# Kernel optimization log

Hardware: AMD Instinct MI355X
Metric: run time of the kernel (lower is better)

Reference implementation:

```python
import jax, jax.numpy as jnp
import numpy as np

B, P, C, O = 16, 19248, 81, 32
POS_THRESH, NEG_THRESH, NEGPOS_RATIO = 0.5, 0.4, 3
BBOX_ALPHA, CONF_ALPHA = 1.5, 1.0
VAR0, VAR1 = 0.1, 0.2  # SSD encoding variances


def setup_inputs() -> dict:
    key = jax.random.key(0)
    ks = jax.random.split(key, 7)
    loc_data = jax.random.normal(ks[0], (B, P, 4), dtype=jnp.float32)
    conf_data = jax.random.normal(ks[1], (B, P, C), dtype=jnp.float32)
    # priors in center form (cx, cy, w, h), all positive
    cxcy = jax.random.uniform(ks[2], (P, 2), minval=0.05, maxval=0.95)
    wh = jax.random.uniform(ks[3], (P, 2), minval=0.05, maxval=0.30)
    priors = jnp.concatenate([cxcy, wh], axis=-1).astype(jnp.float32)
    # gt boxes in point form (x1, y1, x2, y2), valid and inside [0,1]
    gcxcy = jax.random.uniform(ks[4], (B, O, 2), minval=0.1, maxval=0.9)
    gwh = jax.random.uniform(ks[5], (B, O, 2), minval=0.05, maxval=0.4)
    gt_boxes = jnp.clip(jnp.concatenate([gcxcy - gwh / 2, gcxcy + gwh / 2], axis=-1), 0.0, 1.0).astype(jnp.float32)
    gt_labels = jax.random.randint(ks[6], (B, O), 0, C - 1, dtype=jnp.int32)  # 0..79, bg is class 0 after +1
    return {"loc_data": loc_data, "conf_data": conf_data, "priors": priors,
            "gt_boxes": gt_boxes, "gt_labels": gt_labels}


def _point_form(boxes):
    # center form (cx,cy,w,h) -> point form (x1,y1,x2,y2)
    return jnp.concatenate([boxes[:, :2] - boxes[:, 2:] / 2,
                            boxes[:, :2] + boxes[:, 2:] / 2], axis=-1)


def _jaccard(a, b):
    # a: [O,4] point form, b: [P,4] point form -> IoU [O,P]
    lt = jnp.maximum(a[:, None, :2], b[None, :, :2])
    rb = jnp.minimum(a[:, None, 2:], b[None, :, 2:])
    inter = jnp.prod(jnp.clip(rb - lt, 0.0, None), axis=-1)
    area_a = jnp.prod(a[:, 2:] - a[:, :2], axis=-1)[:, None]
    area_b = jnp.prod(b[:, 2:] - b[:, :2], axis=-1)[None, :]
    return inter / (area_a + area_b - inter)


def _encode(matched, priors):
    # matched: [P,4] point form gt; priors: [P,4] center form
    g_cxcy = ((matched[:, :2] + matched[:, 2:]) / 2 - priors[:, :2]) / (VAR0 * priors[:, 2:])
    g_wh = jnp.log((matched[:, 2:] - matched[:, :2]) / priors[:, 2:]) / VAR1
    return jnp.concatenate([g_cxcy, g_wh], axis=-1)


def _match_one(truths, labels, priors):
    # truths: [O,4] point form, labels: [O] int, priors: [P,4] center form
    overlaps = _jaccard(truths, _point_form(priors))          # [O,P]
    best_truth_overlap = overlaps.max(axis=0)                  # [P]
    best_truth_idx = overlaps.argmax(axis=0)                   # [P]
    best_prior_idx = overlaps.argmax(axis=1)                   # [O]
    # ensure every gt is matched to its best prior
    best_truth_overlap = best_truth_overlap.at[best_prior_idx].set(2.0)
    best_truth_idx = best_truth_idx.at[best_prior_idx].set(jnp.arange(truths.shape[0]))
    matched = truths[best_truth_idx]                           # [P,4]
    conf = labels[best_truth_idx] + 1                          # [P]
    conf = jnp.where(best_truth_overlap < POS_THRESH, -1, conf)  # neutral
    conf = jnp.where(best_truth_overlap < NEG_THRESH, 0, conf)   # background
    loc = _encode(matched, priors)                             # [P,4]
    return loc, conf


def _multibox_loss(loc_data, conf_data, priors, gt_boxes, gt_labels):
    loc_t, conf_t = jax.vmap(_match_one, in_axes=(0, 0, None))(gt_boxes, gt_labels, priors)
    pos = conf_t > 0                                           # [B,P]
    # --- localization: smooth L1 on positives ---
    d = jnp.abs(loc_data - loc_t)
    sl1 = jnp.where(d < 1.0, 0.5 * d * d, d - 0.5)
    loss_B = jnp.sum(sl1 * pos[..., None].astype(sl1.dtype)) * BBOX_ALPHA
    # --- OHEM confidence loss ---
    logZ = jax.nn.logsumexp(conf_data, axis=-1)                # [B,P]
    loss_c = logZ - conf_data[..., 0]                          # log_sum_exp - background logit
    loss_c = jnp.where(pos | (conf_t < 0), 0.0, loss_c)
    order = jnp.argsort(-loss_c, axis=1)                       # descending
    idx_rank = jnp.argsort(order, axis=1)                      # rank of each prior
    num_pos = jnp.sum(pos, axis=1, keepdims=True)              # [B,1]
    num_neg = jnp.clip(NEGPOS_RATIO * num_pos, None, P - 1)
    neg = (idx_rank < num_neg) & (~pos) & (conf_t >= 0)
    ce = logZ - jnp.take_along_axis(conf_data, jnp.maximum(conf_t, 0)[..., None], axis=-1)[..., 0]
    loss_C = jnp.sum(ce * (pos | neg).astype(ce.dtype)) * CONF_ALPHA
    total_num_pos = jnp.sum(pos).astype(loc_data.dtype)
    return jnp.stack([loss_B, loss_C]) / total_num_pos


def reference(loc_data, conf_data, priors, gt_boxes, gt_labels):
    return _multibox_loss(loc_data, conf_data, priors, gt_boxes, gt_labels)
```

## Files before the change

### kernel.cpp

```cpp
#include <hip/hip_runtime.h>
#include <math.h>

#define B_ 16
#define P_ 19248
#define C_ 81
#define O_ 32
#define POS_TH 0.5f
#define NEG_TH 0.4f
#define RPB 128
#define TPB 512
#define PQ  4812
#define BP_BLK (B_ * O_ * 4)
#define BT_BPB 76
#define NJ 38

__device__ __forceinline__ float sl1(float x) {
    float d = fabsf(x);
    return (d < 1.0f) ? 0.5f * d * d : d - 0.5f;
}

__device__ __forceinline__ float iou_gt_prior(float4 t, float4 pr) {
    float px1 = pr.x - pr.z * 0.5f;
    float py1 = pr.y - pr.w * 0.5f;
    float px2 = pr.x + pr.z * 0.5f;
    float py2 = pr.y + pr.w * 0.5f;
    float ltx = fmaxf(t.x, px1), lty = fmaxf(t.y, py1);
    float rbx = fminf(t.z, px2), rby = fminf(t.w, py2);
    float iw = fmaxf(rbx - ltx, 0.0f), ih = fmaxf(rby - lty, 0.0f);
    float inter = iw * ih;
    float area_t = (t.z - t.x) * (t.w - t.y);
    float area_p = (px2 - px1) * (py2 - py1);
    return inter / (area_t + area_p - inter);
}

template <int PER>
__device__ __forceinline__ void pick_top(const int* __restrict__ h, int kk, int tid,
                                         int* s_bin, int* s_kk, int* wsum) {
    const int lane = tid & 63, wid = tid >> 6;
    const int base = tid * PER;
    int v[PER]; int s = 0;
    #pragma unroll
    for (int j = 0; j < PER; ++j) { v[j] = h[base + j]; s += v[j]; }
    int x = s;
    #pragma unroll
    for (int d = 1; d < 64; d <<= 1) {
        int y = __shfl_down(x, d);
        if (lane + d < 64) x += y;
    }
    if (lane == 0) wsum[wid] = x;
    __syncthreads();
    int above = 0;
    #pragma unroll
    for (int w = 0; w < 8; ++w) if (w > wid) above += wsum[w];
    int T = (x - s) + above;
    if (T < kk && kk <= T + s) {
        int kl = kk - T, cum = 0;
        #pragma unroll
        for (int j = PER - 1; j >= 0; --j) {
            if (cum + v[j] >= kl) { *s_bin = base + j; *s_kk = kl - cum; break; }
            cum += v[j];
        }
    }
    __syncthreads();
}

template <int PER>
__device__ __forceinline__ void pick_bot(const int* __restrict__ h, int kk, int tid,
                                         int* s_bin, int* s_kk, int* wsum) {
    const int lane = tid & 63, wid = tid >> 6;
    const int base = tid * PER;
    int v[PER]; int s = 0;
    #pragma unroll
    for (int j = 0; j < PER; ++j) { v[j] = h[base + j]; s += v[j]; }
    int x = s;
    #pragma unroll
    for (int d = 1; d < 64; d <<= 1) {
        int y = __shfl_up(x, d);
        if (lane >= d) x += y;
    }
    if (lane == 63) wsum[wid] = x;
    __syncthreads();
    int below = 0;
    #pragma unroll
    for (int w = 0; w < 8; ++w) if (w < wid) below += wsum[w];
    int T = (x - s) + below;
    if (T < kk && kk <= T + s) {
        int kl = kk - T, cum = 0;
        #pragma unroll
        for (int j = 0; j < PER; ++j) {
            if (cum + v[j] >= kl) { *s_bin = base + j; *s_kk = kl - cum; break; }
            cum += v[j];
        }
    }
    __syncthreads();
}

__global__ void k_match(const float* __restrict__ priors,
                        const float* __restrict__ gt_boxes,
                        const int* __restrict__ gt_labels,
                        unsigned long long* __restrict__ best_key,
                        float* __restrict__ bt_ov,
                        int* __restrict__ bt_ix,
                        int* __restrict__ bt_lab) {
    const int bid = blockIdx.x;
    if (bid < BP_BLK) {
        int pair = bid >> 2, qtr = bid & 3;
        int b = pair >> 5, o = pair & 31;
        float4 t = ((const float4*)gt_boxes)[b * O_ + o];
        float bestv = -1.0f; int besti = 0;
        int pstart = qtr * PQ;
        for (int p = pstart + threadIdx.x; p < pstart + PQ; p += 256) {
            float4 pr = ((const float4*)priors)[p];
            float v = iou_gt_prior(t, pr);
            if (v > bestv) { bestv = v; besti = p; }
        }
        __shared__ float sv[256];
        __shared__ int   si[256];
        sv[threadIdx.x] = bestv; si[threadIdx.x] = besti;
        __syncthreads();
        for (int s = 128; s > 0; s >>= 1) {
            if (threadIdx.x < s) {
                float ov = sv[threadIdx.x + s]; int oi = si[threadIdx.x + s];
                if (ov > sv[threadIdx.x] ||
                    (ov == sv[threadIdx.x] && oi < si[threadIdx.x])) {
                    sv[threadIdx.x] = ov; si[threadIdx.x] = oi;
                }
            }
            __syncthreads();
        }
        if (threadIdx.x == 0) {
            unsigned long long key =
                ((unsigned long long)__float_as_uint(sv[0]) << 32) |
                (unsigned long long)(0xFFFFFFFFu - (unsigned int)si[0]);
            atomicMax(&best_key[pair], key);
        }
    } else {
        int idx = bid - BP_BLK;
        int b = idx / BT_BPB;
        int p = (idx % BT_BPB) * 256 + threadIdx.x;
        __shared__ float4 gt[O_];
        __shared__ int    gl[O_];
        if (threadIdx.x < O_) {
            gt[threadIdx.x] = ((const float4*)gt_boxes)[b * O_ + threadIdx.x];
            gl[threadIdx.x] = gt_labels[b * O_ + threadIdx.x];
        }
        __syncthreads();
        if (p >= P_) return;
        float4 pr = ((const float4*)priors)[p];
        float bestv = -1.0f; int besti = 0;
        for (int o = 0; o < O_; ++o) {
            float v = iou_gt_prior(gt[o], pr);
            if (v > bestv) { bestv = v; besti = o; }
        }
        size_t bp = (size_t)b * P_ + p;
        bt_ov[bp] = bestv;
        bt_ix[bp] = besti;
        bt_lab[bp] = gl[besti];
    }
}

__global__ void k_force(const unsigned long long* __restrict__ best_key,
                        const int* __restrict__ gt_labels,
                        float* __restrict__ bt_ov,
                        int* __restrict__ bt_ix,
                        int* __restrict__ bt_lab,
                        int* __restrict__ num_pos,
                        float* __restrict__ accum,
                        int* __restrict__ done) {
    const int tid = threadIdx.x;
    const int b = tid >> 5, o = tid & 31;
    unsigned long long key = best_key[b * O_ + o];
    int p  = (int)(0xFFFFFFFFu - (unsigned int)(key & 0xFFFFFFFFu));
    int ll = gt_labels[b * O_ + o];
    if (tid < B_) num_pos[tid] = 0;
    if (tid == 0) { accum[0] = 0.0f; accum[1] = 0.0f; *done = 0; }
    const int lanebase = tid & 32;
    for (int oo = 0; oo < O_; ++oo) {
        int pp = __shfl(p, lanebase + oo);
        int l2 = __shfl(ll, lanebase + oo);
        if (o == 0) {
            size_t idx = (size_t)b * P_ + pp;
            bt_ov[idx] = 2.0f;
            bt_ix[idx] = oo;
            bt_lab[idx] = l2;
        }
    }
}

__global__ __launch_bounds__(TPB, 6) void
k_main(const float* __restrict__ loc_data,
       const float* __restrict__ conf_data,
       const float* __restrict__ priors,
       const float* __restrict__ gt_boxes,
       const float* __restrict__ bt_ov,
       const int* __restrict__ bt_ix,
       const int* __restrict__ bt_lab,
       float* __restrict__ lossc,
       float* __restrict__ ce_neg,
       int* __restrict__ num_pos,
       float* __restrict__ accum) {
    __shared__ float srow[RPB * C_];
    __shared__ float s_lB, s_ceP;
    __shared__ int s_np0, s_np1;
    const int row0 = blockIdx.x * RPB;
    const int tid = threadIdx.x;
    const int w = tid >> 6;
    if (tid == 0) { s_lB = 0.0f; s_ceP = 0.0f; s_np0 = 0; s_np1 = 0; }

    {
        const float4* src = (const float4*)(conf_data + (size_t)row0 * C_);
        float4* dst4 = (float4*)srow;
        #pragma unroll
        for (int k = 0; k < 5; ++k) {
            __builtin_amdgcn_global_load_lds(
                (const __attribute__((address_space(1))) void*)(src + k * 512 + tid),
                (__attribute__((address_space(3))) void*)(dst4 + k * 512 + (w << 6)),
                16, 0, 0);
        }
        if (tid < 32) {
            __builtin_amdgcn_global_load_lds(
                (const __attribute__((address_space(1))) void*)(src + 2560 + tid),
                (__attribute__((address_space(3))) void*)(dst4 + 2560),
                16, 0, 0);
        }
    }
    __syncthreads();

    const int r = tid >> 2;
    const int q = tid & 3;
    const int bp = row0 + r;
    const int b = bp / P_;
    const int b0 = row0 / P_;
    const int p = bp - b * P_;
    const float* row = srow + r * C_;
    const int j0 = 20 * q;

    float ma = row[j0], mb = row[j0 + 1], mc = row[j0 + 2], md = row[j0 + 3];
    #pragma unroll
    for (int i = 4; i < 20; i += 4) {
        ma = fmaxf(ma, row[j0 + i]);     mb = fmaxf(mb, row[j0 + i + 1]);
        mc = fmaxf(mc, row[j0 + i + 2]); md = fmaxf(md, row[j0 + i + 3]);
    }
    float m = fmaxf(fmaxf(ma, mb), fmaxf(mc, md));
    if (q == 3) m = fmaxf(m, row[80]);
    m = fmaxf(m, __shfl_xor(m, 1));
    m = fmaxf(m, __shfl_xor(m, 2));

    float sa = 0.f, sb = 0.f, sc = 0.f, sd = 0.f;
    #pragma unroll
    for (int i = 0; i < 20; i += 4) {
        sa += __expf(row[j0 + i] - m);     sb += __expf(row[j0 + i + 1] - m);
        sc += __expf(row[j0 + i + 2] - m); sd += __expf(row[j0 + i + 3] - m);
    }
    float s = (sa + sb) + (sc + sd);
    if (q == 3) s += __expf(row[80] - m);
    s += __shfl_xor(s, 1);
    s += __shfl_xor(s, 2);
    float logZ = m + __logf(s);

    if (q == 0) {
        float ov = bt_ov[bp];
        int lab = bt_lab[bp];
        int conf_t = lab + 1;
        if (ov < POS_TH) conf_t = -1;
        if (ov < NEG_TH) conf_t = 0;
        bool pos = conf_t > 0;

        float lc = (pos || conf_t < 0) ? 0.0f : (logZ - row[0]);
        int cls = pos ? conf_t : 0;
        float ce = logZ - row[cls];

        lossc[bp] = lc;
        ce_neg[bp] = (conf_t == 0) ? ce : 0.0f;

        if (pos) {
            int ti = bt_ix[bp];
            float4 t = ((const float4*)gt_boxes)[b * O_ + ti];
            float4 pr = ((const float4*)priors)[p];
            float mcx = (t.x + t.z) * 0.5f;
            float mcy = (t.y + t.w) * 0.5f;
            float gx = (mcx - pr.x) / (0.1f * pr.z);
            float gy = (mcy - pr.y) / (0.1f * pr.w);
            float gw = logf((t.z - t.x) / pr.z) / 0.2f;
            float gh = logf((t.w - t.y) / pr.w) / 0.2f;
            float4 ld = ((const float4*)loc_data)[bp];
            float sc2 = sl1(ld.x - gx) + sl1(ld.y - gy) + sl1(ld.z - gw) + sl1(ld.w - gh);
            atomicAdd(&s_lB, sc2);
            atomicAdd(&s_ceP, ce);
            if (b == b0) atomicAdd(&s_np0, 1); else atomicAdd(&s_np1, 1);
        }
    }
    __syncthreads();
    if (tid == 0) {
        if (s_lB != 0.0f) atomicAdd(&accum[0], s_lB);
        if (s_ceP != 0.0f) atomicAdd(&accum[1], s_ceP);
        if (s_np0) atomicAdd(&num_pos[b0], s_np0);
        if (s_np1) atomicAdd(&num_pos[b0 + 1], s_np1);
    }
}

__global__ __launch_bounds__(512) void
k_ohem(const float* __restrict__ lossc, const float* __restrict__ ce_neg,
       const int* __restrict__ num_pos, const float* __restrict__ accum,
       float* __restrict__ ce_sum, int* __restrict__ done,
       float* __restrict__ out) {
    const int b = blockIdx.x;
    const int tid = threadIdx.x;
    const float* lc = lossc + (size_t)b * P_;
    const float* cn = ce_neg + (size_t)b * P_;
    __shared__ int h[2048];
    __shared__ int wsum[8];
    __shared__ int s_bin, s_kk;
    __shared__ float red[512];

    int k = 3 * num_pos[b];
    if (k > P_ - 1) k = P_ - 1;

    float result = 0.0f;
    if (k > 0) {
        unsigned int fb[NJ]; float cv[NJ];
        #pragma unroll
        for (int j = 0; j < NJ; ++j) {
            int i = tid + j * 512;
            bool valid = (i < P_);
            fb[j] = valid ? __float_as_uint(lc[i]) : 0xFFFFFFFFu;
            cv[j] = valid ? cn[i] : 0.0f;
        }
        for (int i = tid; i < 2048; i += 512) h[i] = 0;
        __syncthreads();
        #pragma unroll
        for (int j = 0; j < NJ; ++j) atomicAdd(&h[fb[j] >> 21], 1);
        __syncthreads();
        pick_top<2>(h, k, tid, &s_bin, &s_kk, wsum);
        const unsigned int T = (unsigned int)s_bin;
        int kk = s_kk;

        for (int i = tid; i < 2048; i += 512) h[i] = 0;
        __syncthreads();
        float sum = 0.0f;
        #pragma unroll
        for (int j = 0; j < NJ; ++j) {
            unsigned int bin = fb[j] >> 21;
            if (bin > T) sum += cv[j];
            else if (bin == T) atomicAdd(&h[(fb[j] >> 10) & 2047], 1);
        }
        __syncthreads();
        pick_top<4>(h, kk, tid, &s_bin, &s_kk, wsum);
        const unsigned int pre21 = (T << 11) | (unsigned int)s_bin;
        kk = s_kk;

        for (int i = tid; i < 1024; i += 512) h[i] = 0;
        __syncthreads();
        #pragma unroll
        for (int j = 0; j < NJ; ++j)
            if ((fb[j] >> 10) == pre21) atomicAdd(&h[fb[j] & 1023], 1);
        __syncthreads();
        pick_top<2>(h, kk, tid, &s_bin, &s_kk, wsum);
        const unsigned int V = (pre21 << 10) | (unsigned int)s_bin;
        const int ee = h[s_bin];
        kk = s_kk;

        if (kk == ee) {
            #pragma unroll
            for (int j = 0; j < NJ; ++j)
                if ((fb[j] >> 21) == T && fb[j] >= V) sum += cv[j];
        } else {
            for (int i = tid; i < 512; i += 512) h[i] = 0;
            __syncthreads();
            #pragma unroll
            for (int j = 0; j < NJ; ++j)
                if (fb[j] == V) atomicAdd(&h[(tid + j * 512) >> 6], 1);
            __syncthreads();
            pick_bot<1>(h, kk, tid, &s_bin, &s_kk, wsum);
            const int d6 = s_bin;
            kk = s_kk;
            h[tid] = 0;
            __syncthreads();
            #pragma unroll
            for (int j = 0; j < NJ; ++j) {
                int i = tid + j * 512;
                if (fb[j] == V && (i >> 6) == d6) atomicAdd(&h[i & 63], 1);
            }
            __syncthreads();
            pick_bot<1>(h, kk, tid, &s_bin, &s_kk, wsum);
            const int Istar = (d6 << 6) | s_bin;
            #pragma unroll
            for (int j = 0; j < NJ; ++j) {
                int i = tid + j * 512;
                if ((fb[j] >> 21) == T && (fb[j] > V || (fb[j] == V && i <= Istar)))
                    sum += cv[j];
            }
        }

        red[tid] = sum;
        __syncthreads();
        for (int s = 256; s > 0; s >>= 1) {
            if (tid < s) red[tid] += red[tid + s];
            __syncthreads();
        }
        result = red[0];
    }

    if (tid == 0) {
        ce_sum[b] = result;
        __threadfence();
        int old = atomicAdd(done, 1);
        if (old == B_ - 1) {
            __threadfence();
            int tp = 0; float ns = 0.0f;
            for (int bb = 0; bb < B_; ++bb) { tp += num_pos[bb]; ns += ce_sum[bb]; }
            float inv = 1.0f / (float)tp;
            out[0] = accum[0] * 1.5f * inv;
            out[1] = (accum[1] + ns) * inv;
        }
    }
}

extern "C" void kernel_launch(void* const* d_in, const int* in_sizes, int n_in,
                              void* d_out, int out_size, void* d_ws, size_t ws_size,
                              hipStream_t stream) {
    const float* loc    = (const float*)d_in[0];
    const float* conf   = (const float*)d_in[1];
    const float* priors = (const float*)d_in[2];
    const float* gtb    = (const float*)d_in[3];
    const int*   gtl    = (const int*)d_in[4];
    float* out = (float*)d_out;

    const size_t BP = (size_t)B_ * P_;
    float* W = (float*)d_ws;
    float* bt_ov   = W;
    float* lossc   = W + BP;
    float* ce_neg  = W + 2 * BP;
    int*   bt_ix   = (int*)(W + 3 * BP);
    int*   bt_lab  = (int*)(W + 4 * BP);
    unsigned long long* best_key = (unsigned long long*)(W + 5 * BP);
    int*   num_pos = (int*)(best_key + B_ * O_);
    float* ce_sum  = (float*)(num_pos + B_);
    float* accum   = ce_sum + B_;
    int*   done    = (int*)(accum + 2);

    hipMemsetAsync(best_key, 0, B_ * O_ * sizeof(unsigned long long), stream);
    hipLaunchKernelGGL(k_match, dim3(BP_BLK + B_ * BT_BPB), dim3(256), 0, stream,
                       priors, gtb, gtl, best_key, bt_ov, bt_ix, bt_lab);
    hipLaunchKernelGGL(k_force, dim3(1), dim3(512), 0, stream,
                       best_key, gtl, bt_ov, bt_ix, bt_lab, num_pos, accum, done);
    hipLaunchKernelGGL(k_main, dim3((int)(BP / RPB)), dim3(TPB), 0, stream,
                       loc, conf, priors, gtb, bt_ov, bt_ix, bt_lab,
                       lossc, ce_neg, num_pos, accum);
    hipLaunchKernelGGL(k_ohem, dim3(B_), dim3(512), 0, stream,
                       lossc, ce_neg, num_pos, accum, ce_sum, done, out);
}
```

Baseline: 119.9 us.

## Fold forced-match kernel into main kernel and widen OHEM select to 1024 threads

Removes the single-block k_force launch. Each k_main block now loads the per-GT best-prior indices and labels for its batch rows into shared memory and applies the forced matches itself. The zeroing of num_pos, accum and done moves into the existing memset. k_ohem now uses 1024 threads with half the per-thread register arrays, and the radix-select histograms and scans are adjusted to match. This saves a serial kernel launch and doubles parallelism in the OHEM selection, at the cost of a 32-entry shared-memory scan per row in k_main and more barrier participants in k_ohem.

```diff
diff --git a/kernel.cpp b/kernel.cpp
--- a/kernel.cpp
+++ b/kernel.cpp
@@ -12,7 +12,8 @@
 #define PQ  4812
 #define BP_BLK (B_ * O_ * 4)
 #define BT_BPB 76
-#define NJ 38
+#define OT 1024
+#define NJ 19
 
 __device__ __forceinline__ float sl1(float x) {
     float d = fabsf(x);
@@ -51,7 +52,7 @@
     __syncthreads();
     int above = 0;
     #pragma unroll
-    for (int w = 0; w < 8; ++w) if (w > wid) above += wsum[w];
+    for (int w = 0; w < 16; ++w) if (w > wid) above += wsum[w];
     int T = (x - s) + above;
     if (T < kk && kk <= T + s) {
         int kl = kk - T, cum = 0;
@@ -82,7 +83,7 @@
     __syncthreads();
     int below = 0;
     #pragma unroll
-    for (int w = 0; w < 8; ++w) if (w < wid) below += wsum[w];
+    for (int w = 0; w < 16; ++w) if (w < wid) below += wsum[w];
     int T = (x - s) + below;
     if (T < kk && kk <= T + s) {
         int kl = kk - T, cum = 0;
@@ -159,39 +160,13 @@
     }
 }
 
-__global__ void k_force(const unsigned long long* __restrict__ best_key,
-                        const int* __restrict__ gt_labels,
-                        float* __restrict__ bt_ov,
-                        int* __restrict__ bt_ix,
-                        int* __restrict__ bt_lab,
-                        int* __restrict__ num_pos,
-                        float* __restrict__ accum,
-                        int* __restrict__ done) {
-    const int tid = threadIdx.x;
-    const int b = tid >> 5, o = tid & 31;
-    unsigned long long key = best_key[b * O_ + o];
-    int p  = (int)(0xFFFFFFFFu - (unsigned int)(key & 0xFFFFFFFFu));
-    int ll = gt_labels[b * O_ + o];
-    if (tid < B_) num_pos[tid] = 0;
-    if (tid == 0) { accum[0] = 0.0f; accum[1] = 0.0f; *done = 0; }
-    const int lanebase = tid & 32;
-    for (int oo = 0; oo < O_; ++oo) {
-        int pp = __shfl(p, lanebase + oo);
-        int l2 = __shfl(ll, lanebase + oo);
-        if (o == 0) {
-            size_t idx = (size_t)b * P_ + pp;
-            bt_ov[idx] = 2.0f;
-            bt_ix[idx] = oo;
-            bt_lab[idx] = l2;
-        }
-    }
-}
-
 __global__ __launch_bounds__(TPB, 6) void
 k_main(const float* __restrict__ loc_data,
        const float* __restrict__ conf_data,
        const float* __restrict__ priors,
        const float* __restrict__ gt_boxes,
+       const int* __restrict__ gt_labels,
+       const unsigned long long* __restrict__ best_key,
        const float* __restrict__ bt_ov,
        const int* __restrict__ bt_ix,
        const int* __restrict__ bt_lab,
@@ -200,9 +175,12 @@
        int* __restrict__ num_pos,
        float* __restrict__ accum) {
     __shared__ float srow[RPB * C_];
+    __shared__ int s_fp[2][O_];
+    __shared__ int s_fl[2][O_];
     __shared__ float s_lB, s_ceP;
     __shared__ int s_np0, s_np1;
     const int row0 = blockIdx.x * RPB;
+    const int b0 = row0 / P_;
     const int tid = threadIdx.x;
     const int w = tid >> 6;
     if (tid == 0) { s_lB = 0.0f; s_ceP = 0.0f; s_np0 = 0; s_np1 = 0; }
@@ -224,13 +202,24 @@
                 16, 0, 0);
         }
     }
+    if (tid < 2 * O_) {
+        int half = tid >> 5, o = tid & 31;
+        int bb = b0 + half;
+        int fp = -1, fl = 0;
+        if (bb < B_) {
+            unsigned long long key = best_key[bb * O_ + o];
+            fp = (int)(0xFFFFFFFFu - (unsigned int)(key & 0xFFFFFFFFu));
+            fl = gt_labels[bb * O_ + o];
+        }
+        s_fp[half][o] = fp;
+        s_fl[half][o] = fl;
+    }
     __syncthreads();
 
     const int r = tid >> 2;
     const int q = tid & 3;
     const int bp = row0 + r;
     const int b = bp / P_;
-    const int b0 = row0 / P_;
     const int p = bp - b * P_;
     const float* row = srow + r * C_;
     const int j0 = 20 * q;
@@ -259,12 +248,26 @@
     float logZ = m + __logf(s);
 
     if (q == 0) {
-        float ov = bt_ov[bp];
-        int lab = bt_lab[bp];
-        int conf_t = lab + 1;
-        if (ov < POS_TH) conf_t = -1;
-        if (ov < NEG_TH) conf_t = 0;
-        bool pos = conf_t > 0;
+        const int whichb = b - b0;
+        int foo = -1;
+        #pragma unroll
+        for (int oo = O_ - 1; oo >= 0; --oo) {
+            if (foo < 0 && s_fp[whichb][oo] == p) foo = oo;
+        }
+        int conf_t, ti = 0;
+        bool pos;
+        if (foo >= 0) {
+            conf_t = s_fl[whichb][foo] + 1;
+            pos = true;
+            ti = foo;
+        } else {
+            float ov = bt_ov[bp];
+            conf_t = bt_lab[bp] + 1;
+            if (ov < POS_TH) conf_t = -1;
+            if (ov < NEG_TH) conf_t = 0;
+            pos = conf_t > 0;
+            if (pos) ti = bt_ix[bp];
+        }
 
         float lc = (pos || conf_t < 0) ? 0.0f : (logZ - row[0]);
         int cls = pos ? conf_t : 0;
@@ -274,7 +277,6 @@
         ce_neg[bp] = (conf_t == 0) ? ce : 0.0f;
 
         if (pos) {
-            int ti = bt_ix[bp];
             float4 t = ((const float4*)gt_boxes)[b * O_ + ti];
             float4 pr = ((const float4*)priors)[p];
             float mcx = (t.x + t.z) * 0.5f;
@@ -299,7 +301,7 @@
     }
 }
 
-__global__ __launch_bounds__(512) void
+__global__ __launch_bounds__(OT) void
 k_ohem(const float* __restrict__ lossc, const float* __restrict__ ce_neg,
        const int* __restrict__ num_pos, const float* __restrict__ accum,
        float* __restrict__ ce_sum, int* __restrict__ done,
@@ -309,9 +311,9 @@
     const float* lc = lossc + (size_t)b * P_;
     const float* cn = ce_neg + (size_t)b * P_;
     __shared__ int h[2048];
-    __shared__ int wsum[8];
+    __shared__ int wsum[16];
     __shared__ int s_bin, s_kk;
-    __shared__ float red[512];
+    __shared__ float red[OT];
 
     int k = 3 * num_pos[b];
     if (k > P_ - 1) k = P_ - 1;
@@ -321,12 +323,12 @@
         unsigned int fb[NJ]; float cv[NJ];
         #pragma unroll
         for (int j = 0; j < NJ; ++j) {
-            int i = tid + j * 512;
+            int i = tid + j * OT;
             bool valid = (i < P_);
-            fb[j] = valid ? __float_as_uint(lc[i]) : 0xFFFFFFFFu;
+            fb[j] = valid ? __float_as_uint(lc[i]) : 0u;
             cv[j] = valid ? cn[i] : 0.0f;
         }
-        for (int i = tid; i < 2048; i += 512) h[i] = 0;
+        h[tid] = 0; h[tid + 1024] = 0;
         __syncthreads();
         #pragma unroll
         for (int j = 0; j < NJ; ++j) atomicAdd(&h[fb[j] >> 21], 1);
@@ -335,7 +337,7 @@
         const unsigned int T = (unsigned int)s_bin;
         int kk = s_kk;
 
-        for (int i = tid; i < 2048; i += 512) h[i] = 0;
+        h[tid] = 0; h[tid + 1024] = 0;
         __syncthreads();
         float sum = 0.0f;
         #pragma unroll
@@ -345,11 +347,11 @@
             else if (bin == T) atomicAdd(&h[(fb[j] >> 10) & 2047], 1);
         }
         __syncthreads();
-        pick_top<4>(h, kk, tid, &s_bin, &s_kk, wsum);
+        pick_top<2>(h, kk, tid, &s_bin, &s_kk, wsum);
         const unsigned int pre21 = (T << 11) | (unsigned int)s_bin;
         kk = s_kk;
 
-        for (int i = tid; i < 1024; i += 512) h[i] = 0;
+        h[tid] = 0; h[tid + 1024] = 0;
         __syncthreads();
         #pragma unroll
         for (int j = 0; j < NJ; ++j)
@@ -365,28 +367,28 @@
             for (int j = 0; j < NJ; ++j)
                 if ((fb[j] >> 21) == T && fb[j] >= V) sum += cv[j];
         } else {
-            for (int i = tid; i < 512; i += 512) h[i] = 0;
+            h[tid] = 0; h[tid + 1024] = 0;
             __syncthreads();
             #pragma unroll
             for (int j = 0; j < NJ; ++j)
-                if (fb[j] == V) atomicAdd(&h[(tid + j * 512) >> 6], 1);
-            __syncthreads();
-            pick_bot<1>(h, kk, tid, &s_bin, &s_kk, wsum);
+                if (fb[j] == V) atomicAdd(&h[(tid + j * OT) >> 6], 1);
+            __syncthreads();
+            pick_bot<2>(h, kk, tid, &s_bin, &s_kk, wsum);
             const int d6 = s_bin;
             kk = s_kk;
-            h[tid] = 0;
+            h[tid] = 0; h[tid + 1024] = 0;
             __syncthreads();
             #pragma unroll
             for (int j = 0; j < NJ; ++j) {
-                int i = tid + j * 512;
+                int i = tid + j * OT;
                 if (fb[j] == V && (i >> 6) == d6) atomicAdd(&h[i & 63], 1);
             }
             __syncthreads();
-            pick_bot<1>(h, kk, tid, &s_bin, &s_kk, wsum);
+            pick_bot<2>(h, kk, tid, &s_bin, &s_kk, wsum);
             const int Istar = (d6 << 6) | s_bin;
             #pragma unroll
             for (int j = 0; j < NJ; ++j) {
-                int i = tid + j * 512;
+                int i = tid + j * OT;
                 if ((fb[j] >> 21) == T && (fb[j] > V || (fb[j] == V && i <= Istar)))
                     sum += cv[j];
             }
@@ -394,7 +396,7 @@
 
         red[tid] = sum;
         __syncthreads();
-        for (int s = 256; s > 0; s >>= 1) {
+        for (int s = OT / 2; s > 0; s >>= 1) {
             if (tid < s) red[tid] += red[tid + s];
             __syncthreads();
         }
@@ -439,14 +441,15 @@
     float* accum   = ce_sum + B_;
     int*   done    = (int*)(accum + 2);
 
-    hipMemsetAsync(best_key, 0, B_ * O_ * sizeof(unsigned long long), stream);
+    size_t zbytes = B_ * O_ * sizeof(unsigned long long) +
+                    B_ * sizeof(int) + B_ * sizeof(float) +
+                    2 * sizeof(float) + sizeof(int);
+    hipMemsetAsync(best_key, 0, zbytes, stream);
     hipLaunchKernelGGL(k_match, dim3(BP_BLK + B_ * BT_BPB), dim3(256), 0, stream,
                        priors, gtb, gtl, best_key, bt_ov, bt_ix, bt_lab);
-    hipLaunchKernelGGL(k_force, dim3(1), dim3(512), 0, stream,
-                       best_key, gtl, bt_ov, bt_ix, bt_lab, num_pos, accum, done);
     hipLaunchKernelGGL(k_main, dim3((int)(BP / RPB)), dim3(TPB), 0, stream,
-                       loc, conf, priors, gtb, bt_ov, bt_ix, bt_lab,
-                       lossc, ce_neg, num_pos, accum);
-    hipLaunchKernelGGL(k_ohem, dim3(B_), dim3(512), 0, stream,
+                       loc, conf, priors, gtb, gtl, best_key,
+                       bt_ov, bt_ix, bt_lab, lossc, ce_neg, num_pos, accum);
+    hipLaunchKernelGGL(k_ohem, dim3(B_), dim3(OT), 0, stream,
                        lossc, ce_neg, num_pos, accum, ce_sum, done, out);
 }
```

Result: no change. 119.0 us (-0.8%).
